# Kernel optimization log

Hardware: AMD Instinct MI355X
Metric: run time of the kernel (lower is better)

## Reference

```python
import jax, jax.numpy as jnp
import numpy as np

N_TARGET = 1_000_000
GRID = 220
C_IN, C_OUT = 32, 64
BN_EPS = 1e-5


def _build_topology():
    # Real sparse-voxel topology: random occupied cells in a GRID^3 volume.
    rng = np.random.default_rng(0)
    raw = rng.integers(0, GRID, size=(1_400_000, 3), dtype=np.int64)
    keys = np.unique((raw[:, 0] * GRID + raw[:, 1]) * GRID + raw[:, 2])[:N_TARGET]
    N = keys.shape[0]
    coords = np.stack([keys // (GRID * GRID), (keys // GRID) % GRID, keys % GRID], axis=1)
    # Rulebook: for each of the 27 kernel offsets, index of the neighbor voxel (N = missing -> zero pad row).
    nbr = np.full((N, 27), N, dtype=np.int32)
    k = 0
    for dx in (-1, 0, 1):
        for dy in (-1, 0, 1):
            for dz in (-1, 0, 1):
                nc = coords + np.array([dx, dy, dz])
                valid = np.all((nc >= 0) & (nc < GRID), axis=1)
                nk = (nc[:, 0] * GRID + nc[:, 1]) * GRID + nc[:, 2]
                pos = np.clip(np.searchsorted(keys, nk), 0, N - 1)
                found = valid & (keys[pos] == nk)
                nbr[found, k] = pos[found].astype(np.int32)
                k += 1
    # MaxPool(2,2): voxels sharing coords//2 pool together.
    PG = GRID // 2 + 1
    pkeys = ((coords[:, 0] // 2) * PG + coords[:, 1] // 2) * PG + coords[:, 2] // 2
    uniq, pool_ids = np.unique(pkeys, return_inverse=True)
    return N, nbr, pool_ids.astype(np.int32), int(uniq.shape[0])


def setup_inputs() -> dict:
    N, nbr, pool_ids, num_pooled = _build_topology()
    key = jax.random.key(0)
    k1, k2, k3 = jax.random.split(key, 3)
    return {
        "feats": jax.random.normal(k1, (N, C_IN), dtype=jnp.float32),
        "W1": jax.random.normal(k2, (27, C_IN, C_OUT), dtype=jnp.float32) * 0.1,
        "gamma1": jnp.ones((C_OUT,), jnp.float32),
        "beta1": jnp.zeros((C_OUT,), jnp.float32),
        "W2": jax.random.normal(k3, (27, C_OUT, C_OUT), dtype=jnp.float32) * 0.1,
        "gamma2": jnp.ones((C_OUT,), jnp.float32),
        "beta2": jnp.zeros((C_OUT,), jnp.float32),
        "nbr_idx": jnp.asarray(nbr),
        "pool_ids": jnp.asarray(pool_ids),
        "num_pooled": num_pooled,
    }


def _sparse_conv3(f, W, nbr_idx):
    # f: [N, Cin], W: [27, Cin, Cout], nbr_idx: [N, 27] with pad index N.
    N = f.shape[0]
    fp = jnp.concatenate([f, jnp.zeros((1, f.shape[1]), f.dtype)], axis=0)  # zero pad row
    out = jnp.zeros((N, W.shape[2]), f.dtype)
    for k in range(27):  # fixed kernel offsets: gather -> GEMM -> accumulate
        out = out + fp[nbr_idx[:, k]] @ W[k]
    return out


def _batch_norm(f, gamma, beta):
    # Training-mode BN over the voxel dim (biased variance), as torch BatchNorm.
    m = f.mean(axis=0)
    v = f.var(axis=0)
    return (f - m) * jax.lax.rsqrt(v + BN_EPS) * gamma + beta


def reference(feats, W1, gamma1, beta1, W2, gamma2, beta2, nbr_idx, pool_ids, num_pooled):
    x = jax.nn.relu(_batch_norm(_sparse_conv3(feats, W1, nbr_idx), gamma1, beta1))
    x = _batch_norm(_sparse_conv3(x, W2, nbr_idx), gamma2, beta2)
    pooled = jax.ops.segment_max(x, pool_ids, num_segments=num_pooled)
    return x, pooled
```

## Files before the change

kernel.cpp:

```cpp
#include <hip/hip_runtime.h>
#include <hip/hip_bf16.h>
#include <stdint.h>

#define TPB 256

typedef __bf16 bf16x8 __attribute__((ext_vector_type(8)));
typedef float f32x4 __attribute__((ext_vector_type(4)));
union U16x8 { uint4 u; bf16x8 b; };

typedef const uint32_t __attribute__((address_space(1))) glb_u32;
typedef uint32_t __attribute__((address_space(3))) lds_u32;

__device__ __forceinline__ float bfbits2f(uint32_t lo16) {
  union { uint32_t u; float f; } c; c.u = lo16 << 16; return c.f;
}
__device__ __forceinline__ uint16_t f2bf_rne(float f) {
  union { float f; uint32_t u; } c; c.f = f;
  uint32_t r = 0x7FFFu + ((c.u >> 16) & 1u);
  return (uint16_t)((c.u + r) >> 16);
}

__global__ __launch_bounds__(TPB) void prep_w_kernel(
    const float* __restrict__ W1, const float* __restrict__ W2,
    uint16_t* __restrict__ w1t, uint16_t* __restrict__ w2t)
{
  int i = blockIdx.x * TPB + threadIdx.x;
  if (i < 27 * 2048) {
    int k = i >> 11, cin = (i >> 6) & 31, cout = i & 63;
    int cin2 = (((cin >> 3) ^ (cout & 3)) << 3) | (cin & 7);
    w1t[(k << 11) + (cout << 5) + cin2] = f2bf_rne(W1[i]);
  } else {
    int j = i - 27 * 2048;
    if (j < 27 * 4096) {
      int k = j >> 12, cin = (j >> 6) & 63, cout = j & 63;
      int cin2 = (((cin >> 3) ^ (cout & 7)) << 3) | (cin & 7);
      w2t[(k << 12) + (cout << 6) + cin2] = f2bf_rne(W2[j]);
    }
  }
}

__global__ __launch_bounds__(TPB) void prep_x0_kernel(
    const float* __restrict__ feats, uint16_t* __restrict__ x0, long long N)
{
  long long t = (long long)blockIdx.x * TPB + threadIdx.x;
  if (t >= (N + 1) * 4) return;
  long long e = t * 8;
  uint4 o;
  if (e < N * 32) {
    float4 a = *(const float4*)(feats + e);
    float4 b = *(const float4*)(feats + e + 4);
    o.x = (uint32_t)f2bf_rne(a.x) | ((uint32_t)f2bf_rne(a.y) << 16);
    o.y = (uint32_t)f2bf_rne(a.z) | ((uint32_t)f2bf_rne(a.w) << 16);
    o.z = (uint32_t)f2bf_rne(b.x) | ((uint32_t)f2bf_rne(b.y) << 16);
    o.w = (uint32_t)f2bf_rne(b.z) | ((uint32_t)f2bf_rne(b.w) << 16);
  } else {
    o.x = o.y = o.z = o.w = 0;
  }
  *(uint4*)(x0 + e) = o;
}

__global__ __launch_bounds__(TPB) void bucket_build_kernel(
    const int* __restrict__ pool_ids, int* __restrict__ count,
    int* __restrict__ members, long long N)
{
  long long i = (long long)blockIdx.x * TPB + threadIdx.x;
  if (i < N) {
    int pid = pool_ids[i];
    int slot = atomicAdd(&count[pid], 1);
    members[(long long)pid * 8 + slot] = (int)i;
  }
}

template <int CIN, int R>
__global__ __launch_bounds__(TPB, 4) void conv_mfma_kernel(
    const uint16_t* __restrict__ x, const uint16_t* __restrict__ wt,
    const int* __restrict__ nbr, uint16_t* __restrict__ yb,
    float* __restrict__ statsrep, int N)
{
  constexpr int CHUNKS = CIN / 32;
  constexpr int LOGROWB = (CIN == 32) ? 6 : 7;
  constexpr int SWZ = (CIN == 32) ? 3 : 7;
  constexpr int WKB = 64 * CIN * 2;
  constexpr int NW = WKB / (TPB * 16);
  constexpr int ROWS = 4 * R * 16;
  constexpr int NINTS = ROWS * 27;
  constexpr int NCH16 = NINTS / 4;

  __shared__ __align__(16) char Wlds[2][WKB];
  __shared__ __align__(16) int nbrLds[NINTS];
  __shared__ float sred[4][128];

  const int tid = threadIdx.x;
  const int lane = tid & 63;
  const int wave = tid >> 6;
  const int l15 = lane & 15;
  const int l4 = lane >> 4;

  int bid;
  {
    int nwg = gridDim.x, q = nwg >> 3, r = nwg & 7;
    int xcd = blockIdx.x & 7, pos = blockIdx.x >> 3;
    bid = (xcd < r ? xcd * (q + 1) : r * (q + 1) + (xcd - r) * q) + pos;
  }
  const long long row0 = (long long)bid * ROWS;

  f32x4 acc[R][4];
#pragma unroll
  for (int r = 0; r < R; ++r)
#pragma unroll
    for (int t = 0; t < 4; ++t)
      acc[r][t] = (f32x4){0.f, 0.f, 0.f, 0.f};

  {
    const char* nsrc = (const char*)nbr + row0 * 108;
    long long blkB = (long long)N * 108 - row0 * 108;
    int fullChunks = (int)(blkB >> 4);
    if (fullChunks > NCH16) fullChunks = NCH16;
#pragma unroll
    for (int u = 0; u < (NCH16 + TPB - 1) / TPB; ++u) {
      int idx = u * TPB + tid;
      if (idx < fullChunks)
        __builtin_amdgcn_global_load_lds((glb_u32*)(nsrc + idx * 16),
                                         (lds_u32*)((char*)nbrLds + idx * 16), 16, 0, 0);
    }
    for (int ii = fullChunks * 4 + tid; ii < NINTS; ii += TPB) {
      long long gi = row0 * 27 + ii;
      nbrLds[ii] = (gi < (long long)N * 27) ? nbr[gi] : N;
    }
  }

  auto stageW = [&](int k, int b) {
    const char* src = (const char*)(wt + (size_t)k * 64 * CIN);
#pragma unroll
    for (int u = 0; u < NW; ++u) {
      int off = (tid + u * TPB) * 16;
      __builtin_amdgcn_global_load_lds((glb_u32*)(src + off),
                                       (lds_u32*)(&Wlds[b][off]), 16, 0, 0);
    }
  };
  auto gather = [&](int k, U16x8 (&dst)[R][CHUNKS]) -> int {
    int m = 0;
#pragma unroll
    for (int r = 0; r < R; ++r) {
      int lrow = (wave * R + r) * 16 + l15;
      int g = nbrLds[lrow * 27 + k];
      if (__any(g < N)) {
        const uint16_t* xr = x + (size_t)g * CIN + (l4 << 3);
#pragma unroll
        for (int c = 0; c < CHUNKS; ++c)
          dst[r][c].u = *(const uint4*)(xr + c * 32);
        m |= 1 << r;
      }
    }
    return m;
  };
  auto compute = [&](int wsel, U16x8 (&xs)[R][CHUNKS], int mask) {
    bf16x8 bfrag[4][CHUNKS];
#pragma unroll
    for (int t = 0; t < 4; ++t) {
      int n = t * 16 + l15;
#pragma unroll
      for (int c = 0; c < CHUNKS; ++c) {
        int colb = (l4 << 4) + (c << 6);
        int d = (n << LOGROWB) | (colb ^ ((n & SWZ) << 4));
        U16x8 tmp; tmp.u = *(const uint4*)(&Wlds[wsel][d]);
        bfrag[t][c] = tmp.b;
      }
    }
#pragma unroll
    for (int r = 0; r < R; ++r) {
      if (mask & (1 << r)) {
#pragma unroll
        for (int c = 0; c < CHUNKS; ++c)
#pragma unroll
          for (int t = 0; t < 4; ++t)
            acc[r][t] = __builtin_amdgcn_mfma_f32_16x16x32_bf16(
                xs[r][c].b, bfrag[t][c], acc[r][t], 0, 0, 0);
      }
    }
  };

  U16x8 xA[R][CHUNKS], xB[R][CHUNKS];
  int maskA, maskB;

  stageW(0, 0);
  __syncthreads();
  maskA = gather(0, xA);

#pragma unroll 1
  for (int kk = 0; kk < 13; ++kk) {
    if (kk > 0) __syncthreads();
    stageW(2 * kk + 1, 1);
    maskB = gather(2 * kk + 1, xB);
    compute(0, xA, maskA);
    __syncthreads();
    if (2 * kk + 2 < 27) {
      stageW(2 * kk + 2, 0);
      maskA = gather(2 * kk + 2, xA);
    }
    compute(1, xB, maskB);
  }
  __syncthreads();
  compute(0, xA, maskA);

#pragma unroll
  for (int r = 0; r < R; ++r) {
    long long vr0 = row0 + (wave * R + r) * 16 + (l4 << 2);
#pragma unroll
    for (int reg = 0; reg < 4; ++reg) {
      long long vr = vr0 + reg;
      if (vr < N) {
        uint16_t* yr = yb + vr * 64 + l15;
#pragma unroll
        for (int t = 0; t < 4; ++t) yr[t * 16] = f2bf_rne(acc[r][t][reg]);
      }
    }
  }

  float s[4], s2[4];
#pragma unroll
  for (int t = 0; t < 4; ++t) { s[t] = 0.f; s2[t] = 0.f; }
#pragma unroll
  for (int r = 0; r < R; ++r) {
    long long vr0 = row0 + (wave * R + r) * 16 + (l4 << 2);
#pragma unroll
    for (int reg = 0; reg < 4; ++reg) {
      if (vr0 + reg < N) {
#pragma unroll
        for (int t = 0; t < 4; ++t) {
          float v = acc[r][t][reg];
          s[t] += v;
          s2[t] = fmaf(v, v, s2[t]);
        }
      }
    }
  }
#pragma unroll
  for (int t = 0; t < 4; ++t) {
    s[t] += __shfl_xor(s[t], 16);
    s[t] += __shfl_xor(s[t], 32);
    s2[t] += __shfl_xor(s2[t], 16);
    s2[t] += __shfl_xor(s2[t], 32);
  }
  __syncthreads();
  if (l4 == 0) {
#pragma unroll
    for (int t = 0; t < 4; ++t) {
      sred[wave][t * 16 + l15] = s[t];
      sred[wave][64 + t * 16 + l15] = s2[t];
    }
  }
  __syncthreads();
  if (tid < 128) {
    float tot = sred[0][tid] + sred[1][tid] + sred[2][tid] + sred[3][tid];
    atomicAdd(&statsrep[(bid & 15) * 128 + tid], tot);
  }
}

__global__ void bn_finalize_kernel(const float* __restrict__ reps,
                                   float* __restrict__ fin, float n)
{
  int c = threadIdx.x;
  float s = 0.f, s2 = 0.f;
  for (int r = 0; r < 16; ++r) { s += reps[r * 128 + c]; s2 += reps[r * 128 + 64 + c]; }
  float mean = s / n;
  float var = s2 / n - mean * mean;
  fin[c] = mean;
  fin[64 + c] = rsqrtf(var + 1e-5f);
}

__global__ __launch_bounds__(TPB) void bn_relu_bf16_kernel(
    const uint16_t* __restrict__ yb, const float* __restrict__ fin,
    const float* __restrict__ gamma, const float* __restrict__ beta,
    uint16_t* __restrict__ x1, long long N)
{
  long long e = ((long long)blockIdx.x * TPB + threadIdx.x) * 8;
  if (e >= (N + 1) * 64) return;
  long long row = e >> 6;
  int c = (int)(e & 63);
  uint4 out;
  if (row < N) {
    uint4 v = *(const uint4*)(yb + e);
    const uint32_t vv[4] = {v.x, v.y, v.z, v.w};
    uint32_t res[4];
#pragma unroll
    for (int q = 0; q < 4; ++q) {
      int cc = c + q * 2;
      float a0 = bfbits2f(vv[q] & 0xFFFFu);
      float a1 = bfbits2f(vv[q] >> 16);
      float o0 = fmaf((a0 - fin[cc]) * fin[64 + cc], gamma[cc], beta[cc]);
      float o1 = fmaf((a1 - fin[cc + 1]) * fin[64 + cc + 1], gamma[cc + 1], beta[cc + 1]);
      o0 = o0 > 0.f ? o0 : 0.f;
      o1 = o1 > 0.f ? o1 : 0.f;
      res[q] = (uint32_t)f2bf_rne(o0) | ((uint32_t)f2bf_rne(o1) << 16);
    }
    out.x = res[0]; out.y = res[1]; out.z = res[2]; out.w = res[3];
  } else {
    out.x = out.y = out.z = out.w = 0;
  }
  *(uint4*)(x1 + e) = out;
}

__global__ __launch_bounds__(TPB) void pool_max_kernel(
    const uint16_t* __restrict__ yb, const float* __restrict__ fin,
    const float* __restrict__ gamma, const float* __restrict__ beta,
    const int* __restrict__ count, const int* __restrict__ members,
    float* __restrict__ pooled, long long P)
{
  long long pid = (long long)blockIdx.x * 16 + (threadIdx.x >> 4);
  if (pid >= P) return;
  int c0 = (threadIdx.x & 15) * 4;
  float4 m = *(const float4*)(fin + c0);
  float4 r = *(const float4*)(fin + 64 + c0);
  float4 g = *(const float4*)(gamma + c0);
  float4 b = *(const float4*)(beta + c0);
  int cnt = count[pid];
  float4 acc = {-3.4e38f, -3.4e38f, -3.4e38f, -3.4e38f};
  const int* mem = members + pid * 8;
  for (int t = 0; t < cnt; ++t) {
    long long row = mem[t];
    ushort4 v = *(const ushort4*)(yb + row * 64 + c0);
    acc.x = fmaxf(acc.x, fmaf((bfbits2f(v.x) - m.x) * r.x, g.x, b.x));
    acc.y = fmaxf(acc.y, fmaf((bfbits2f(v.y) - m.y) * r.y, g.y, b.y));
    acc.z = fmaxf(acc.z, fmaf((bfbits2f(v.z) - m.z) * r.z, g.z, b.z));
    acc.w = fmaxf(acc.w, fmaf((bfbits2f(v.w) - m.w) * r.w, g.w, b.w));
  }
  *(float4*)(pooled + pid * 64 + c0) = acc;
}

__global__ __launch_bounds__(TPB) void bn_write_kernel(
    const uint16_t* __restrict__ yb, const float* __restrict__ fin,
    const float* __restrict__ gamma, const float* __restrict__ beta,
    float* __restrict__ xout, long long N)
{
  long long e = ((long long)blockIdx.x * TPB + threadIdx.x) * 8;
  if (e >= N * 64) return;
  int c = (int)(e & 63);
  uint4 v = *(const uint4*)(yb + e);
  const uint32_t vv[4] = {v.x, v.y, v.z, v.w};
  float o[8];
#pragma unroll
  for (int q = 0; q < 4; ++q) {
    int cc = c + q * 2;
    float a0 = bfbits2f(vv[q] & 0xFFFFu);
    float a1 = bfbits2f(vv[q] >> 16);
    o[q * 2 + 0] = fmaf((a0 - fin[cc]) * fin[64 + cc], gamma[cc], beta[cc]);
    o[q * 2 + 1] = fmaf((a1 - fin[cc + 1]) * fin[64 + cc + 1], gamma[cc + 1], beta[cc + 1]);
  }
  float4 lo = {o[0], o[1], o[2], o[3]};
  float4 hi = {o[4], o[5], o[6], o[7]};
  *(float4*)(xout + e) = lo;
  *(float4*)(xout + e + 4) = hi;
}

extern "C" void kernel_launch(void* const* d_in, const int* in_sizes, int n_in,
                              void* d_out, int out_size, void* d_ws, size_t ws_size,
                              hipStream_t stream)
{
  const float* feats  = (const float*)d_in[0];
  const float* W1     = (const float*)d_in[1];
  const float* gamma1 = (const float*)d_in[2];
  const float* beta1  = (const float*)d_in[3];
  const float* W2     = (const float*)d_in[4];
  const float* gamma2 = (const float*)d_in[5];
  const float* beta2  = (const float*)d_in[6];
  const int* nbr      = (const int*)d_in[7];
  const int* pool_ids = (const int*)d_in[8];

  const long long N = (long long)in_sizes[0] / 32;
  const long long P = (long long)out_size / 64 - N;

  char* ws = (char*)d_ws;
  uint16_t* yb = (uint16_t*)ws;
  size_t y_bytes = ((size_t)N * 64 * 2 + 255) & ~(size_t)255;
  char* regB = ws + y_bytes;
  size_t regB_bytes = ((size_t)(N + 1) * 64 * 2 + 255) & ~(size_t)255;
  uint16_t* x0 = (uint16_t*)regB;
  uint16_t* x1 = (uint16_t*)regB;
  float* reps1 = (float*)(regB + regB_bytes);
  float* reps2 = reps1 + 16 * 128;
  float* fin1 = reps2 + 16 * 128;
  float* fin2 = fin1 + 128;

  float* xout = (float*)d_out;
  float* pooled = xout + (size_t)N * 64;
  int* count   = (int*)xout;
  int* members = count + P;
  uint16_t* w1t = (uint16_t*)pooled;
  uint16_t* w2t = w1t + 27 * 2048;

  hipMemsetAsync(reps1, 0, 2 * 16 * 128 * sizeof(float), stream);
  hipMemsetAsync(count, 0, (size_t)P * 4, stream);

  prep_w_kernel<<<(27 * 2048 + 27 * 4096 + TPB - 1) / TPB, TPB, 0, stream>>>(W1, W2, w1t, w2t);
  prep_x0_kernel<<<(int)(((N + 1) * 4 + TPB - 1) / TPB), TPB, 0, stream>>>(feats, x0, N);
  bucket_build_kernel<<<(int)((N + TPB - 1) / TPB), TPB, 0, stream>>>(pool_ids, count, members, N);

  const int convBlocks = (int)((N + 127) / 128);
  conv_mfma_kernel<32, 2><<<convBlocks, TPB, 0, stream>>>(x0, w1t, nbr, yb, reps1, (int)N);
  bn_finalize_kernel<<<1, 64, 0, stream>>>(reps1, fin1, (float)N);

  long long t1 = ((N + 1) * 64) / 8;
  bn_relu_bf16_kernel<<<(int)((t1 + TPB - 1) / TPB), TPB, 0, stream>>>(
      yb, fin1, gamma1, beta1, x1, N);

  conv_mfma_kernel<64, 2><<<convBlocks, TPB, 0, stream>>>(x1, w2t, nbr, yb, reps2, (int)N);
  bn_finalize_kernel<<<1, 64, 0, stream>>>(reps2, fin2, (float)N);

  pool_max_kernel<<<(int)((P + 15) / 16), TPB, 0, stream>>>(
      yb, fin2, gamma2, beta2, count, members, pooled, P);

  long long t2 = (N * 64) / 8;
  bn_write_kernel<<<(int)((t2 + TPB - 1) / TPB), TPB, 0, stream>>>(
      yb, fin2, gamma2, beta2, xout, N);
}
```

Before: 726.4 us.

## Deepen conv pipeline to four weight slots and fuse BN write into pooling

The conv kernel now keeps four LDS weight slots and processes kernel offsets two at a time, with two gathers in flight per stage. It drops the per-row skip of empty neighbors so MFMAs always run, and sets a separate occupancy bound per conv instantiation (3 for the 64-channel case). The final BN write is folded into the pool-max kernel, which writes each member row's normalized output while taking the max, removing one full pass over yb. The count/members buckets move from the output buffer into workspace so the fused kernel can write xout without clobbering them. In exchange the conv uses more LDS and registers, which may lower occupancy, and all-missing neighbor tiles are no longer skipped.

```diff
diff --git a/kernel.cpp b/kernel.cpp
--- a/kernel.cpp
+++ b/kernel.cpp
@@ -71,8 +71,8 @@
   }
 }
 
-template <int CIN, int R>
-__global__ __launch_bounds__(TPB, 4) void conv_mfma_kernel(
+template <int CIN, int R, int OCC>
+__global__ __launch_bounds__(TPB, OCC) void conv_mfma_kernel(
     const uint16_t* __restrict__ x, const uint16_t* __restrict__ wt,
     const int* __restrict__ nbr, uint16_t* __restrict__ yb,
     float* __restrict__ statsrep, int N)
@@ -86,7 +86,7 @@
   constexpr int NINTS = ROWS * 27;
   constexpr int NCH16 = NINTS / 4;
 
-  __shared__ __align__(16) char Wlds[2][WKB];
+  __shared__ __align__(16) char Wlds[4][WKB];
   __shared__ __align__(16) int nbrLds[NINTS];
   __shared__ float sred[4][128];
 
@@ -129,32 +129,27 @@
     }
   }
 
-  auto stageW = [&](int k, int b) {
+  auto stageW = [&](int k, int slot) {
     const char* src = (const char*)(wt + (size_t)k * 64 * CIN);
 #pragma unroll
     for (int u = 0; u < NW; ++u) {
       int off = (tid + u * TPB) * 16;
       __builtin_amdgcn_global_load_lds((glb_u32*)(src + off),
-                                       (lds_u32*)(&Wlds[b][off]), 16, 0, 0);
+                                       (lds_u32*)(&Wlds[slot][off]), 16, 0, 0);
     }
   };
-  auto gather = [&](int k, U16x8 (&dst)[R][CHUNKS]) -> int {
-    int m = 0;
+  auto gather = [&](int k, U16x8 (&dst)[R][CHUNKS]) {
 #pragma unroll
     for (int r = 0; r < R; ++r) {
       int lrow = (wave * R + r) * 16 + l15;
       int g = nbrLds[lrow * 27 + k];
-      if (__any(g < N)) {
-        const uint16_t* xr = x + (size_t)g * CIN + (l4 << 3);
-#pragma unroll
-        for (int c = 0; c < CHUNKS; ++c)
-          dst[r][c].u = *(const uint4*)(xr + c * 32);
-        m |= 1 << r;
-      }
-    }
-    return m;
+      const uint16_t* xr = x + (size_t)g * CIN + (l4 << 3);
+#pragma unroll
+      for (int c = 0; c < CHUNKS; ++c)
+        dst[r][c].u = *(const uint4*)(xr + c * 32);
+    }
   };
-  auto compute = [&](int wsel, U16x8 (&xs)[R][CHUNKS], int mask) {
+  auto compute = [&](int slot, U16x8 (&xs)[R][CHUNKS]) {
     bf16x8 bfrag[4][CHUNKS];
 #pragma unroll
     for (int t = 0; t < 4; ++t) {
@@ -163,45 +158,47 @@
       for (int c = 0; c < CHUNKS; ++c) {
         int colb = (l4 << 4) + (c << 6);
         int d = (n << LOGROWB) | (colb ^ ((n & SWZ) << 4));
-        U16x8 tmp; tmp.u = *(const uint4*)(&Wlds[wsel][d]);
+        U16x8 tmp; tmp.u = *(const uint4*)(&Wlds[slot][d]);
         bfrag[t][c] = tmp.b;
       }
     }
 #pragma unroll
-    for (int r = 0; r < R; ++r) {
-      if (mask & (1 << r)) {
-#pragma unroll
-        for (int c = 0; c < CHUNKS; ++c)
-#pragma unroll
-          for (int t = 0; t < 4; ++t)
-            acc[r][t] = __builtin_amdgcn_mfma_f32_16x16x32_bf16(
-                xs[r][c].b, bfrag[t][c], acc[r][t], 0, 0, 0);
-      }
-    }
+    for (int r = 0; r < R; ++r)
+#pragma unroll
+      for (int c = 0; c < CHUNKS; ++c)
+#pragma unroll
+        for (int t = 0; t < 4; ++t)
+          acc[r][t] = __builtin_amdgcn_mfma_f32_16x16x32_bf16(
+              xs[r][c].b, bfrag[t][c], acc[r][t], 0, 0, 0);
   };
 
-  U16x8 xA[R][CHUNKS], xB[R][CHUNKS];
-  int maskA, maskB;
-
-  stageW(0, 0);
-  __syncthreads();
-  maskA = gather(0, xA);
+  U16x8 xPe[R][CHUNKS], xPo[R][CHUNKS], xQe[R][CHUNKS], xQo[R][CHUNKS];
+
+  stageW(0, 0); stageW(1, 1);
+  __syncthreads();
+  gather(0, xPe); gather(1, xPo);
 
 #pragma unroll 1
-  for (int kk = 0; kk < 13; ++kk) {
-    if (kk > 0) __syncthreads();
-    stageW(2 * kk + 1, 1);
-    maskB = gather(2 * kk + 1, xB);
-    compute(0, xA, maskA);
+  for (int t = 0; t < 6; ++t) {
+    const int k4 = 4 * t;
     __syncthreads();
-    if (2 * kk + 2 < 27) {
-      stageW(2 * kk + 2, 0);
-      maskA = gather(2 * kk + 2, xA);
-    }
-    compute(1, xB, maskB);
-  }
-  __syncthreads();
-  compute(0, xA, maskA);
+    stageW(k4 + 2, 2); stageW(k4 + 3, 3);
+    gather(k4 + 2, xQe); gather(k4 + 3, xQo);
+    compute(0, xPe);
+    compute(1, xPo);
+    __syncthreads();
+    stageW(k4 + 4, 0); stageW(k4 + 5, 1);
+    gather(k4 + 4, xPe); gather(k4 + 5, xPo);
+    compute(2, xQe);
+    compute(3, xQo);
+  }
+  __syncthreads();
+  stageW(26, 2);
+  gather(26, xQe);
+  compute(0, xPe);
+  compute(1, xPo);
+  __syncthreads();
+  compute(2, xQe);
 
 #pragma unroll
   for (int r = 0; r < R; ++r) {
@@ -301,11 +298,11 @@
   *(uint4*)(x1 + e) = out;
 }
 
-__global__ __launch_bounds__(TPB) void pool_max_kernel(
+__global__ __launch_bounds__(TPB) void pool_max_write_kernel(
     const uint16_t* __restrict__ yb, const float* __restrict__ fin,
     const float* __restrict__ gamma, const float* __restrict__ beta,
     const int* __restrict__ count, const int* __restrict__ members,
-    float* __restrict__ pooled, long long P)
+    float* __restrict__ xout, float* __restrict__ pooled, long long P)
 {
   long long pid = (long long)blockIdx.x * 16 + (threadIdx.x >> 4);
   if (pid >= P) return;
@@ -320,37 +317,18 @@
   for (int t = 0; t < cnt; ++t) {
     long long row = mem[t];
     ushort4 v = *(const ushort4*)(yb + row * 64 + c0);
-    acc.x = fmaxf(acc.x, fmaf((bfbits2f(v.x) - m.x) * r.x, g.x, b.x));
-    acc.y = fmaxf(acc.y, fmaf((bfbits2f(v.y) - m.y) * r.y, g.y, b.y));
-    acc.z = fmaxf(acc.z, fmaf((bfbits2f(v.z) - m.z) * r.z, g.z, b.z));
-    acc.w = fmaxf(acc.w, fmaf((bfbits2f(v.w) - m.w) * r.w, g.w, b.w));
+    float4 o;
+    o.x = fmaf((bfbits2f(v.x) - m.x) * r.x, g.x, b.x);
+    o.y = fmaf((bfbits2f(v.y) - m.y) * r.y, g.y, b.y);
+    o.z = fmaf((bfbits2f(v.z) - m.z) * r.z, g.z, b.z);
+    o.w = fmaf((bfbits2f(v.w) - m.w) * r.w, g.w, b.w);
+    *(float4*)(xout + row * 64 + c0) = o;
+    acc.x = fmaxf(acc.x, o.x);
+    acc.y = fmaxf(acc.y, o.y);
+    acc.z = fmaxf(acc.z, o.z);
+    acc.w = fmaxf(acc.w, o.w);
   }
   *(float4*)(pooled + pid * 64 + c0) = acc;
-}
-
-__global__ __launch_bounds__(TPB) void bn_write_kernel(
-    const uint16_t* __restrict__ yb, const float* __restrict__ fin,
-    const float* __restrict__ gamma, const float* __restrict__ beta,
-    float* __restrict__ xout, long long N)
-{
-  long long e = ((long long)blockIdx.x * TPB + threadIdx.x) * 8;
-  if (e >= N * 64) return;
-  int c = (int)(e & 63);
-  uint4 v = *(const uint4*)(yb + e);
-  const uint32_t vv[4] = {v.x, v.y, v.z, v.w};
-  float o[8];
-#pragma unroll
-  for (int q = 0; q < 4; ++q) {
-    int cc = c + q * 2;
-    float a0 = bfbits2f(vv[q] & 0xFFFFu);
-    float a1 = bfbits2f(vv[q] >> 16);
-    o[q * 2 + 0] = fmaf((a0 - fin[cc]) * fin[64 + cc], gamma[cc], beta[cc]);
-    o[q * 2 + 1] = fmaf((a1 - fin[cc + 1]) * fin[64 + cc + 1], gamma[cc + 1], beta[cc + 1]);
-  }
-  float4 lo = {o[0], o[1], o[2], o[3]};
-  float4 hi = {o[4], o[5], o[6], o[7]};
-  *(float4*)(xout + e) = lo;
-  *(float4*)(xout + e + 4) = hi;
 }
 
 extern "C" void kernel_launch(void* const* d_in, const int* in_sizes, int n_in,
@@ -381,11 +359,11 @@
   float* reps2 = reps1 + 16 * 128;
   float* fin1 = reps2 + 16 * 128;
   float* fin2 = fin1 + 128;
+  int* count   = (int*)(fin2 + 128);
+  int* members = count + P;
 
   float* xout = (float*)d_out;
   float* pooled = xout + (size_t)N * 64;
-  int* count   = (int*)xout;
-  int* members = count + P;
   uint16_t* w1t = (uint16_t*)pooled;
   uint16_t* w2t = w1t + 27 * 2048;
 
@@ -397,20 +375,16 @@
   bucket_build_kernel<<<(int)((N + TPB - 1) / TPB), TPB, 0, stream>>>(pool_ids, count, members, N);
 
   const int convBlocks = (int)((N + 127) / 128);
-  conv_mfma_kernel<32, 2><<<convBlocks, TPB, 0, stream>>>(x0, w1t, nbr, yb, reps1, (int)N);
+  conv_mfma_kernel<32, 2, 4><<<convBlocks, TPB, 0, stream>>>(x0, w1t, nbr, yb, reps1, (int)N);
   bn_finalize_kernel<<<1, 64, 0, stream>>>(reps1, fin1, (float)N);
 
   long long t1 = ((N + 1) * 64) / 8;
   bn_relu_bf16_kernel<<<(int)((t1 + TPB - 1) / TPB), TPB, 0, stream>>>(
       yb, fin1, gamma1, beta1, x1, N);
 
-  conv_mfma_kernel<64, 2><<<convBlocks, TPB, 0, stream>>>(x1, w2t, nbr, yb, reps2, (int)N);
+  conv_mfma_kernel<64, 2, 3><<<convBlocks, TPB, 0, stream>>>(x1, w2t, nbr, yb, reps2, (int)N);
   bn_finalize_kernel<<<1, 64, 0, stream>>>(reps2, fin2, (float)N);
 
-  pool_max_kernel<<<(int)((P + 15) / 16), TPB, 0, stream>>>(
-      yb, fin2, gamma2, beta2, count, members, pooled, P);
-
-  long long t2 = (N * 64) / 8;
-  bn_write_kernel<<<(int)((t2 + TPB - 1) / TPB), TPB, 0, stream>>>(
-      yb, fin2, gamma2, beta2, xout, N);
-}
+  pool_max_write_kernel<<<(int)((P + 15) / 16), TPB, 0, stream>>>(
+      yb, fin2, gamma2, beta2, count, members, xout, pooled, P);
+}
```

Measured after the change: 706.2 us. 2.8% less time.
